# Kernel tuning notes

Measured on AMD Instinct MI355X. Metric: run time of the kernel, lower is better.

## Reference

```python
import jax, jax.numpy as jnp
import numpy as np
from jax import lax

B, F_BINS, T = 4, 128, 16384
J_T, N_W, KF, KT = 4, 8, 33, 129


def setup_inputs() -> dict:
    key = jax.random.key(0)
    k1, k2, k3 = jax.random.split(key, 3)
    x = jax.random.normal(k1, (B, F_BINS, T), dtype=jnp.float32)
    # complex Morlet-style wavelet bank parameters: [J_t, n_w, kf, kt]
    wav_real = jax.random.normal(k2, (J_T, N_W, KF, KT), dtype=jnp.float32) * 0.05
    wav_imag = jax.random.normal(k3, (J_T, N_W, KF, KT), dtype=jnp.float32) * 0.05
    return {"x": x, "wav_real": wav_real, "wav_imag": wav_imag}


def _avg_pool_last(x, w):
    # non-overlapping mean pooling along the last (time) axis, stride == window
    if w == 1:
        return x
    shp = x.shape
    return x.reshape(shp[:-1] + (shp[-1] // w, w)).mean(axis=-1)


def reference(x, wav_real, wav_imag):
    # x: [B, F, T]; wav_real/wav_imag: [J_t, n_w, kf, kt]
    J_t, n_w = wav_real.shape[0], wav_real.shape[1]
    # avg_win_t cascade: 2**J_t halving each octave -> [16, 8, 4, 2]
    avg_wins_t = [2 ** (J_t - j) for j in range(J_t)]
    xi = x[:, None]  # [B, 1, F, T_cur]
    octaves = []
    for j in range(J_t):
        # stack real and imag kernels as 2*n_w output channels of one conv2d
        k = jnp.concatenate([wav_real[j], wav_imag[j]], axis=0)[:, None]  # [2*n_w, 1, kf, kt]
        o = lax.conv_general_dilated(
            xi, k, window_strides=(1, 1), padding='SAME',
            dimension_numbers=('NCHW', 'OIHW', 'NCHW'))  # [B, 2*n_w, F, T_cur]
        # complex modulus (x is real, kernel complex): |conv_r + i*conv_i|
        mod = jnp.sqrt(o[:, :n_w] ** 2 + o[:, n_w:] ** 2)  # [B, n_w, F, T_cur]
        w = avg_wins_t[j]
        octaves.append(_avg_pool_last(mod, w))  # [B, n_w, F, T//2**J_t]
        if w > 1:
            xi = _avg_pool_last(xi, 2)  # decimate input in time by 2
    # all octaves share the same pooled time length -> concat on channel dim
    return jnp.concatenate(octaves, axis=1)  # [B, J_t*n_w, F, T//2**J_t]
```

## Files before the change

### kernel.cpp

```cpp
#include <hip/hip_runtime.h>
#include <math.h>

#define B_      4
#define F_BINS  128
#define T_FULL  16384
#define NW      8
#define KF      33
#define KT      129

#define TT      128
#define ROWS    260
#define PITCH   72
#define DTP     136
#define D2      48

typedef __attribute__((ext_vector_type(8))) short short8;
typedef __attribute__((ext_vector_type(4))) float f32x4;
typedef uint uint4a16 __attribute__((ext_vector_type(4), aligned(16)));

union ABFrag { uint4a16 u; short8 v; };

__device__ __forceinline__ ushort f2bf(float v) {
  unsigned u = __float_as_uint(v);
  unsigned r = (u + 0x7FFFu + ((u >> 16) & 1u)) >> 16;
  return (ushort)r;
}

__device__ __forceinline__ short8 load_a16(const ushort* p) {
  ABFrag f; f.u = *(const uint4a16*)p; return f.v;
}

__device__ __forceinline__ short8 mkG(short8 a, short8 b) {
  return __builtin_shufflevector(a, b, 4, 5, 6, 7, 8, 9, 10, 11);
}

__global__ __launch_bounds__(256) void prep_w(
    const float* __restrict__ wr, const float* __restrict__ wi,
    ushort* __restrict__ wq) {
  int idx = blockIdx.x * 256 + threadIdx.x;
  int d2  = idx % D2;
  int dt  = (idx / D2) % DTP;
  int ch  = (idx / (D2 * DTP)) % 16;
  int gam = (idx / (D2 * DTP * 16)) % 4;
  int oct = idx / (D2 * DTP * 16 * 4);
  int df  = d2 - 4 - gam;
  float v = 0.f;
  if (df >= 0 && df < KF && dt < KT) {
    const float* src = (ch < 8) ? wr : wi;
    v = src[(((size_t)oct * 8 + (ch & 7)) * KF + df) * KT + dt];
  }
  wq[idx] = f2bf(v);
}

__global__ __launch_bounds__(256) void prep_x(
    const float* __restrict__ x,
    ushort* __restrict__ xT0, ushort* __restrict__ xT1,
    ushort* __restrict__ xT2, ushort* __restrict__ xT3) {
  __shared__ float lt[128 * 65];
  const int b  = blockIdx.y;
  const int t0 = blockIdx.x * 64;
  const int tid = threadIdx.x;
  const int wv = tid >> 6, lane = tid & 63;
#pragma unroll
  for (int rep = 0; rep < 32; ++rep) {
    int f = rep * 4 + wv;
    lt[f * 65 + lane] = x[((size_t)b * 128 + f) * T_FULL + t0 + lane];
  }
  __syncthreads();
  ushort* dst[4] = {xT0, xT1, xT2, xT3};
  const int Ts[4] = {16384, 8192, 4096, 2048};
  for (int lvl = 0; lvl < 4; ++lvl) {
    int nt = 64 >> lvl, w = 1 << lvl;
    float inv = 1.f / (float)w;
    int tasks = nt * 16;
    for (int i = tid; i < tasks; i += 256) {
      int tl = i >> 4, fc = i & 15;
      __align__(16) ushort vs[8];
#pragma unroll
      for (int e = 0; e < 8; ++e) {
        float a = 0.f;
        for (int m = 0; m < w; ++m) a += lt[(fc * 8 + e) * 65 + tl * w + m];
        vs[e] = f2bf(a * inv);
      }
      ushort* pdst = dst[lvl] + ((size_t)b * Ts[lvl] + (t0 >> lvl) + tl) * 128 + fc * 8;
      *(uint4*)pdst = *(const uint4*)vs;
    }
  }
}

template<int WP, int OCT>
__global__ __launch_bounds__(256, 3) void conv_mfma(
    const ushort* __restrict__ xT, const ushort* __restrict__ wq,
    float* __restrict__ out, int Tj) {
  __shared__ ushort xt[ROWS * PITCH];
  const int tid = threadIdx.x;
  const int t0 = blockIdx.x * TT;
  const int f0 = blockIdx.y * 32;
  const int b  = blockIdx.z;

  for (int i = tid; i < ROWS * 8; i += 256) {
    int row = i >> 3, fc = i & 7;
    int t = t0 - 64 + row;
    int f = f0 - 16 + fc * 8;
    uint4 v = make_uint4(0u, 0u, 0u, 0u);
    if (t >= 0 && t < Tj && f >= 0 && f < 128)
      v = *(const uint4*)(xT + ((size_t)b * Tj + t) * 128 + f);
    *(uint4*)&xt[row * PITCH + fc * 8] = v;
  }
  __syncthreads();

  const int wave = tid >> 6, lane = tid & 63;
  const int p = lane & 15;
  const int g = lane >> 4;

  const float invw = 1.f / (float)WP;

  for (int gamma = 0; gamma < 4; ++gamma) {
    const ushort* wbase = wq + ((((size_t)OCT * 4 + gamma) * 16 + p) * DTP + g) * D2;
    const ushort* wp = wbase + 4 * D2;
    int rb = (p + g) * PITCH + wave * (32 * PITCH);

    f32x4 acc[8][2];
#pragma unroll
    for (int k = 0; k < 8; ++k)
#pragma unroll
      for (int r = 0; r < 2; ++r) { f32x4 z = {0.f, 0.f, 0.f, 0.f}; acc[k][r] = z; }

    short8 F[6], G[5];
#pragma unroll
    for (int u = 0; u < 6; ++u) F[u] = load_a16(wbase + 8 * u);
    G[0] = mkG(F[0], F[1]);
    G[1] = mkG(F[1], F[2]);

#pragma unroll 1
    for (int c = 0; c < 33; ++c) {
      __builtin_amdgcn_s_setprio(1);
      const int SLO[8] = {0, 0, 1, 1, 2, 2, 3, 3};
#pragma unroll
      for (int s = 0; s < 8; ++s) {
        if (s == 0) G[2] = mkG(F[2], F[3]);
        if (s == 1) G[3] = mkG(F[3], F[4]);
        if (s == 2) G[4] = mkG(F[4], F[5]);
        short8 bv0 = *(const short8*)&xt[rb + s * 8];
        short8 bv1 = *(const short8*)&xt[rb + 16 * PITCH + s * 8];
#pragma unroll
        for (int k = 0; k < 8; ++k) {
          if (s >= SLO[k] && s <= SLO[k] + 4) {
            const int idx = s - SLO[k];
            short8 a = (k & 1) ? F[idx] : G[idx];
            acc[k][0] = __builtin_amdgcn_mfma_f32_16x16x32_bf16(a, bv0, acc[k][0], 0, 0, 0);
            acc[k][1] = __builtin_amdgcn_mfma_f32_16x16x32_bf16(a, bv1, acc[k][1], 0, 0, 0);
          }
        }
        if (s >= 3) F[s - 3] = load_a16(wp + 8 * (s - 3));
        if (s == 6) G[0] = mkG(F[0], F[1]);
        if (s == 7) G[1] = mkG(F[1], F[2]);
      }
      F[5] = load_a16(wp + 40);
      __builtin_amdgcn_s_setprio(0);
      wp += 4 * D2;
      rb += 4 * PITCH;
    }

#pragma unroll
    for (int k = 0; k < 8; ++k) {
      const int fo = f0 + gamma + 4 * k;
#pragma unroll
      for (int fr = 0; fr < 2; ++fr) {
        const int tbase = t0 + 32 * wave + 16 * fr;
#pragma unroll
        for (int r = 0; r < 4; ++r) {
          float a = acc[k][fr][r];
          float o = __shfl_xor(a, 32);
          float m = sqrtf(a * a + o * o);
#pragma unroll
          for (int mask = WP / 2; mask >= 1; mask >>= 1)
            m += __shfl_xor(m, mask);
          if (((p & (WP - 1)) == 0) && g < 2) {
            int ch = 4 * g + r;
            int tcol = (tbase + p) / WP;
            out[(((size_t)b * 32 + OCT * 8 + ch) * 128 + fo) * 1024 + tcol] = m * invw;
          }
        }
      }
    }
  }
}

extern "C" void kernel_launch(void* const* d_in, const int* in_sizes, int n_in,
                              void* d_out, int out_size, void* d_ws, size_t ws_size,
                              hipStream_t stream) {
  const float* x  = (const float*)d_in[0];
  const float* wr = (const float*)d_in[1];
  const float* wi = (const float*)d_in[2];
  float* out = (float*)d_out;

  ushort* xT0 = (ushort*)d_ws;
  ushort* xT1 = xT0 + (size_t)4 * 16384 * 128;
  ushort* xT2 = xT1 + (size_t)4 * 8192 * 128;
  ushort* xT3 = xT2 + (size_t)4 * 4096 * 128;
  ushort* wq  = xT3 + (size_t)4 * 2048 * 128;

  prep_w<<<1671168 / 256, 256, 0, stream>>>(wr, wi, wq);
  prep_x<<<dim3(T_FULL / 64, B_), 256, 0, stream>>>(x, xT0, xT1, xT2, xT3);

  conv_mfma<16, 0><<<dim3(16384 / TT, 4, 4), 256, 0, stream>>>(xT0, wq, out, 16384);
  conv_mfma< 8, 1><<<dim3( 8192 / TT, 4, 4), 256, 0, stream>>>(xT1, wq, out, 8192);
  conv_mfma< 4, 2><<<dim3( 4096 / TT, 4, 4), 256, 0, stream>>>(xT2, wq, out, 4096);
  conv_mfma< 2, 3><<<dim3( 2048 / TT, 4, 4), 256, 0, stream>>>(xT3, wq, out, 2048);
}
```

Measured before the change: 1.834 ms.

## Merge four per-octave conv launches into one flat grid with packed epilogue

Replaces the four templated per-octave conv launches with one 3840-block launch that decodes octave, time tile, frequency block and batch from the flat block index. This removes launch gaps and lets tail blocks of one octave overlap with the others. The epilogue also uses all lanes: upper and lower halves each compute the modulus for different channel rows, which halves the shuffle-reduction work and uses two stores per lane. The cost is that the pooling width is now a runtime value, adding branches and losing compile-time specialization.

```diff
diff --git a/kernel.cpp b/kernel.cpp
--- a/kernel.cpp
+++ b/kernel.cpp
@@ -88,15 +88,28 @@
   }
 }
 
-template<int WP, int OCT>
 __global__ __launch_bounds__(256, 3) void conv_mfma(
-    const ushort* __restrict__ xT, const ushort* __restrict__ wq,
-    float* __restrict__ out, int Tj) {
+    const ushort* __restrict__ xT0, const ushort* __restrict__ xT1,
+    const ushort* __restrict__ xT2, const ushort* __restrict__ xT3,
+    const ushort* __restrict__ wq, float* __restrict__ out) {
   __shared__ ushort xt[ROWS * PITCH];
   const int tid = threadIdx.x;
-  const int t0 = blockIdx.x * TT;
-  const int f0 = blockIdx.y * 32;
-  const int b  = blockIdx.z;
+  const int bx = blockIdx.x;
+
+  int oct, local;
+  if (bx < 2048)      { oct = 0; local = bx; }
+  else if (bx < 3072) { oct = 1; local = bx - 2048; }
+  else if (bx < 3584) { oct = 2; local = bx - 3072; }
+  else                { oct = 3; local = bx - 3584; }
+  const ushort* xT = (oct == 0) ? xT0 : (oct == 1) ? xT1 : (oct == 2) ? xT2 : xT3;
+  const int Tj = T_FULL >> oct;
+  const int lw = 4 - oct;
+  const int nxs = 7 - oct;
+  const int tx = local & ((1 << nxs) - 1);
+  const int rest = local >> nxs;
+  const int t0 = tx * TT;
+  const int f0 = (rest & 3) * 32;
+  const int b  = rest >> 2;
 
   for (int i = tid; i < ROWS * 8; i += 256) {
     int row = i >> 3, fc = i & 7;
@@ -112,11 +125,11 @@
   const int wave = tid >> 6, lane = tid & 63;
   const int p = lane & 15;
   const int g = lane >> 4;
-
-  const float invw = 1.f / (float)WP;
+  const int hi = (lane >= 32);
+  const float invw = 1.0f / (float)(1 << lw);
 
   for (int gamma = 0; gamma < 4; ++gamma) {
-    const ushort* wbase = wq + ((((size_t)OCT * 4 + gamma) * 16 + p) * DTP + g) * D2;
+    const ushort* wbase = wq + ((((size_t)oct * 4 + gamma) * 16 + p) * DTP + g) * D2;
     const ushort* wp = wbase + 4 * D2;
     int rb = (p + g) * PITCH + wave * (32 * PITCH);
 
@@ -168,19 +181,25 @@
 #pragma unroll
       for (int fr = 0; fr < 2; ++fr) {
         const int tbase = t0 + 32 * wave + 16 * fr;
+        float sq[4];
 #pragma unroll
         for (int r = 0; r < 4; ++r) {
           float a = acc[k][fr][r];
           float o = __shfl_xor(a, 32);
-          float m = sqrtf(a * a + o * o);
-#pragma unroll
-          for (int mask = WP / 2; mask >= 1; mask >>= 1)
-            m += __shfl_xor(m, mask);
-          if (((p & (WP - 1)) == 0) && g < 2) {
-            int ch = 4 * g + r;
-            int tcol = (tbase + p) / WP;
-            out[(((size_t)b * 32 + OCT * 8 + ch) * 128 + fo) * 1024 + tcol] = m * invw;
-          }
+          sq[r] = a * a + o * o;
+        }
+        float m0 = sqrtf(hi ? sq[2] : sq[0]);
+        float m1 = sqrtf(hi ? sq[3] : sq[1]);
+        if (lw == 4) { m0 += __shfl_xor(m0, 8); m1 += __shfl_xor(m1, 8); }
+        if (lw >= 3) { m0 += __shfl_xor(m0, 4); m1 += __shfl_xor(m1, 4); }
+        if (lw >= 2) { m0 += __shfl_xor(m0, 2); m1 += __shfl_xor(m1, 2); }
+        m0 += __shfl_xor(m0, 1);  m1 += __shfl_xor(m1, 1);
+        if ((p & ((1 << lw) - 1)) == 0) {
+          const int ch0 = 4 * (g & 1) + (hi ? 2 : 0);
+          const int tcol = (tbase + p) >> lw;
+          size_t o0 = (((size_t)b * 32 + oct * 8 + ch0) * 128 + fo) * 1024 + tcol;
+          out[o0] = m0 * invw;
+          out[o0 + (size_t)128 * 1024] = m1 * invw;
         }
       }
     }
@@ -204,8 +223,5 @@
   prep_w<<<1671168 / 256, 256, 0, stream>>>(wr, wi, wq);
   prep_x<<<dim3(T_FULL / 64, B_), 256, 0, stream>>>(x, xT0, xT1, xT2, xT3);
 
-  conv_mfma<16, 0><<<dim3(16384 / TT, 4, 4), 256, 0, stream>>>(xT0, wq, out, 16384);
-  conv_mfma< 8, 1><<<dim3( 8192 / TT, 4, 4), 256, 0, stream>>>(xT1, wq, out, 8192);
-  conv_mfma< 4, 2><<<dim3( 4096 / TT, 4, 4), 256, 0, stream>>>(xT2, wq, out, 4096);
-  conv_mfma< 2, 3><<<dim3( 2048 / TT, 4, 4), 256, 0, stream>>>(xT3, wq, out, 2048);
-}
+  conv_mfma<<<3840, 256, 0, stream>>>(xT0, xT1, xT2, xT3, wq, out);
+}
```

New measurement: 1.599 ms. -12.9%, faster.
